# Performance work log

Hardware: AMD Instinct MI355X
Metric: run time of the kernel (lower is better)

The kernel has to match this reference:

```python
import jax, jax.numpy as jnp
from jax import lax
import numpy as np

GAMMA = 1.0
N, M = 4096, 4096


def setup_inputs() -> dict:
    key = jax.random.key(0)
    D = jax.random.normal(key, (N, M), dtype=jnp.float32)
    return {"D": D}


def reference(D):
    # Faithful translation of the original forward.
    # Step 1: the module overwrites D with exp(-D/gamma); the DP then runs on E.
    E = jnp.exp(-D / GAMMA)  # [N, M]

    # Step 2: hard-min DP (torch.min, despite the "Soft" name):
    #   c[i,j] = E[i,j] + min(c[i-1,j], c[i,j-1], c[i-1,j-1])
    # Row-wise vectorization: within row i, with a[j] = min(prev[j], prev[j-1])
    # (a[0] = prev[0]), the within-row recursion c[j] = E[j] + min(a[j], c[j-1])
    # unrolls to   c[j] = S[j] + cummin(a - S_shift)[j],  S = cumsum(E_row).
    row0 = jnp.cumsum(E[0])  # first row: pure left-to-right accumulation

    def step(prev, e_row):
        a = jnp.minimum(prev, jnp.concatenate([prev[:1], prev[:-1]]))
        S = jnp.cumsum(e_row)
        Sm1 = jnp.concatenate([jnp.zeros((1,), e_row.dtype), S[:-1]])
        c = S + lax.cummin(a - Sm1)
        return c, None

    last_row, _ = lax.scan(step, row0, E[1:])
    cost = last_row[-1]  # acc_cost[N-1, M-1]

    # Step 3: acc_grad. In the original row-major loop, acc_grad[i,j] is still 0
    # when cell (i,j) is processed (all writers come later), so each cell
    # simply (a) subtracts d[i,j]/gamma from itself and (b) adds d[i,j]/gamma to
    # its (i-1,j-1), (i-1,j), (i,j-1) neighbors, with d = exp(-E/gamma).
    # Fully vectorizable as a shifted stencil:
    d = jnp.exp(-E / GAMMA)
    dp = jnp.pad(d, ((0, 1), (0, 1)))  # zero-pad bottom/right for boundary cells
    acc_grad = (dp[1:, 1:] + dp[1:, :-1] + dp[:-1, 1:] - d) / GAMMA

    return cost, acc_grad
```

## Files before the change

kernel.cpp:

```cpp
#include <hip/hip_runtime.h>
#include <math.h>

#define NN 4096
#define STRIPS 32
#define SW 128
#define RING_ROWS 256
#define RINGB (RING_ROWS * SW * 4)
#define BATCH 32
#define NBATCH 130
#define PAD 64
#define COLPITCH (NN + 2 * PAD)
#define INFV 1e30f
#define SENTU 0xFFFFFFFFu

__device__ __forceinline__ float dpp_wave_shr1(float x) {
    return __int_as_float(__builtin_amdgcn_update_dpp(
        0, __float_as_int(x), 0x138 , 0xf, 0xf, false));
}

__device__ __forceinline__ float bload(const unsigned* colL, int row, int lane) {
    float v = INFV;
    const int rowc = (row < NN) ? row : (NN - 1);
    if (lane < 32) {
        unsigned u = __hip_atomic_load(colL + rowc, __ATOMIC_RELAXED,
                                       __HIP_MEMORY_SCOPE_AGENT);
        v = __uint_as_float(u);
    }
    return v;
}

__device__ __forceinline__ bool has_sent(float b, int rb, int lane) {
    return __any((lane < 32) && ((rb + lane) < NN) &&
                 (__float_as_uint(b) == SENTU));
}

__device__ __forceinline__ void stageB(const float* Sg, float* ring, int rb,
                                       int lane) {
    #pragma unroll
    for (int k = 0; k < 16; ++k) {
        const int r0 = rb + 2 * k;
        const int r0c = (r0 < NN - 1) ? r0 : (NN - 2);
        const int slot = r0 & (RING_ROWS - 1);
        const float* gsrc =
            Sg + (size_t)(r0c + (lane >> 5)) * NN + ((lane & 31) << 2);
        __builtin_amdgcn_global_load_lds(
            (const __attribute__((address_space(1))) unsigned*)gsrc,
            (__attribute__((address_space(3))) unsigned*)((char*)ring +
                                                         slot * (SW * 4)),
            16, 0, 0);
    }
}

template <int DOEXP>
__global__ __launch_bounds__(128, 1) void dtw_dp(const float* __restrict__ S,
                                                 float* __restrict__ cost_out,
                                                 unsigned* __restrict__ colbuf) {
    __shared__ float ring[RING_ROWS * SW];
    __shared__ float inbox[2][32];
    __shared__ float outbox[2][32];
    __shared__ float outdummy[64];

    const int tid = threadIdx.x;
    const int lane = tid & 63;
    const int b = blockIdx.x;
    const int g = ((b & 7) << 2) | (b >> 3);

    const float* Sg = S + g * SW;
    const unsigned* colL = colbuf + (size_t)(g - 1) * COLPITCH + PAD;
    unsigned* colM = colbuf + (size_t)g * COLPITCH + PAD;

    if (tid < 64) {
        {
            const float4 z = make_float4(0.f, 0.f, 0.f, 0.f);
            float4* r4 = reinterpret_cast<float4*>(&ring[192 * SW]);
            #pragma unroll
            for (int i = 0; i < 32; ++i) r4[i * 64 + lane] = z;
        }
        asm volatile("s_waitcnt lgkmcnt(0)" ::: "memory");
        __builtin_amdgcn_s_barrier();

        const bool lane0 = (lane == 0);
        const int ostep = (lane == 63) ? 1 : 0;
        float cur0 = INFV, cur1 = INFV;
        float l1s = INFV, l2s = INFV;
        float bprevc = INFV;
        float save = 0.f;

        unsigned caddr = ((unsigned)((0 - lane) & (RING_ROWS - 1)) << 9) |
                         ((unsigned)lane << 3);

        float2 rvA[BATCH], rvB[BATCH];
        #pragma unroll
        for (int s = 0; s < BATCH; ++s)
            rvA[s] = *reinterpret_cast<const float2*>(
                (const char*)ring + ((caddr + s * 512) & (RINGB - 1)));

#define CSTEP(CUR, NXT, NIDX) do {                                            \
        const int n_ = (NIDX);                                                \
        const float binb = inbox[n_ & 1][lane & 31];                          \
        _Pragma("unroll")                                                     \
        for (int s = 0; s < BATCH; ++s)                                       \
            NXT[s] = *reinterpret_cast<const float2*>(                        \
                (const char*)ring +                                           \
                ((caddr + 16384u + (unsigned)(s * 512)) & (RINGB - 1)));      \
        __builtin_amdgcn_sched_barrier(0);                                    \
        float* obp = (lane == 63) ? &outbox[n_ & 1][0] : &outdummy[lane];     \
        float pbc = INFV;                                                     \
        _Pragma("unroll")                                                     \
        for (int s = 0; s < BATCH; ++s) {                                     \
            float e0, e1;                                                     \
            if (DOEXP) { e0 = __expf(-CUR[s].x); e1 = __expf(-CUR[s].y); }    \
            else       { e0 = CUR[s].x;          e1 = CUR[s].y; }             \
            float bcur;                                                       \
            if (g == 0)                                                       \
                bcur = (n_ == 0 && s == 0) ? 0.f : INFV;                      \
            else                                                              \
                bcur = __int_as_float(                                        \
                    __builtin_amdgcn_readlane(__float_as_int(binb), s));      \
            const float bpv =                                                 \
                (g == 0) ? INFV : ((s == 0) ? bprevc : pbc);                  \
            const float L1 = lane0 ? bcur : l1s;                              \
            const float L2 = lane0 ? bpv : l2s;                               \
            const float m0 = fminf(fminf(L1, cur0), L2);                      \
            const float c0 = e0 + m0;                                         \
            const float c1 = e1 + fminf(c0, fminf(cur0, cur1));               \
            *obp = c1;                                                        \
            obp += ostep;                                                     \
            const float sh = dpp_wave_shr1(c1);                               \
            l2s = l1s; l1s = sh;                                              \
            cur0 = c0; cur1 = c1;                                             \
            pbc = bcur;                                                       \
            if (s == 30) save = c1;                                           \
        }                                                                     \
        bprevc = pbc;                                                         \
        caddr = (caddr + 16384u) & (RINGB - 1);                               \
        asm volatile("s_waitcnt lgkmcnt(0)" ::: "memory");                    \
        __builtin_amdgcn_s_barrier();                                         \
    } while (0)

        for (int i = 0; i < NBATCH / 2; ++i) {
            CSTEP(rvA, rvB, 2 * i);
            CSTEP(rvB, rvA, 2 * i + 1);
        }
#undef CSTEP

        if (g == STRIPS - 1 && lane == 63) cost_out[0] = save;
    } else {
        stageB(Sg, ring, 0, lane);
        stageB(Sg, ring, 32, lane);
        float qv = INFV;
        if (g > 0) {
            qv = bload(colL, lane & 31, lane);
            while (has_sent(qv, 0, lane)) qv = bload(colL, lane & 31, lane);
            if (lane < 32) inbox[0][lane] = qv;
            qv = bload(colL, 32 + (lane & 31), lane);
        }
        asm volatile("s_waitcnt vmcnt(0) lgkmcnt(0)" ::: "memory");
        __builtin_amdgcn_s_barrier();

        for (int n = 0; n < NBATCH; ++n) {
            const int tb = n << 5;
            if (g > 0) {
                const int vb = tb + 32;
                while (has_sent(qv, vb, lane))
                    qv = bload(colL, vb + (lane & 31), lane);
                if (lane < 32) inbox[(n + 1) & 1][lane] = qv;
                qv = bload(colL, tb + 64 + (lane & 31), lane);
            }
            if (n > 0 && lane < 32) {
                const int row = ((n - 1) << 5) - 63 + lane;
                __hip_atomic_store(colM + row,
                                   __float_as_uint(outbox[(n - 1) & 1][lane]),
                                   __ATOMIC_RELAXED, __HIP_MEMORY_SCOPE_AGENT);
            }
            stageB(Sg, ring, tb + 64, lane);
            __builtin_amdgcn_sched_barrier(0);
            if (g > 0) asm volatile("s_waitcnt vmcnt(18)" ::: "memory");
            else       asm volatile("s_waitcnt vmcnt(17)" ::: "memory");
            __builtin_amdgcn_sched_barrier(0);
            asm volatile("s_waitcnt lgkmcnt(0)" ::: "memory");
            __builtin_amdgcn_s_barrier();
        }
        if (lane < 32) {
            const int row = ((NBATCH - 1) << 5) - 63 + lane;
            __hip_atomic_store(colM + row,
                               __float_as_uint(outbox[(NBATCH - 1) & 1][lane]),
                               __ATOMIC_RELAXED, __HIP_MEMORY_SCOPE_AGENT);
        }
    }
}

__global__ __launch_bounds__(256) void eg_kernel(const float* __restrict__ D,
                                                 float* __restrict__ E,
                                                 float* __restrict__ G) {
    const int idx = blockIdx.x * 256 + threadIdx.x;
    const int i = idx >> 10;
    const int j = (idx & 1023) << 2;
    if (i >= NN) return;

    const float* row0 = D + (size_t)i * NN + j;
    const bool hasR = (i + 1) < NN;
    const bool hasC = (j + 4) < NN;

    const float4 r0 = *reinterpret_cast<const float4*>(row0);
    float4 r1 = make_float4(0.f, 0.f, 0.f, 0.f);
    if (hasR) r1 = *reinterpret_cast<const float4*>(row0 + NN);
    const float s0 = hasC ? row0[4] : 0.f;
    const float s1 = (hasR && hasC) ? row0[NN + 4] : 0.f;

    const float ex0 = __expf(-r0.x), ex1 = __expf(-r0.y);
    const float ex2 = __expf(-r0.z), ex3 = __expf(-r0.w);
    *reinterpret_cast<float4*>(E + (size_t)i * NN + j) =
        make_float4(ex0, ex1, ex2, ex3);

    const float a0 = __expf(-ex0), a1 = __expf(-ex1);
    const float a2 = __expf(-ex2), a3 = __expf(-ex3);
    const float a4 = hasC ? __expf(-__expf(-s0)) : 0.f;
    const float b0 = hasR ? __expf(-__expf(-r1.x)) : 0.f;
    const float b1 = hasR ? __expf(-__expf(-r1.y)) : 0.f;
    const float b2 = hasR ? __expf(-__expf(-r1.z)) : 0.f;
    const float b3 = hasR ? __expf(-__expf(-r1.w)) : 0.f;
    const float b4 = (hasR && hasC) ? __expf(-__expf(-s1)) : 0.f;

    float* go = G + (size_t)i * NN + j;
    go[0] = b1 + b0 + a1 - a0;
    go[1] = b2 + b1 + a2 - a1;
    go[2] = b3 + b2 + a3 - a2;
    go[3] = b4 + b3 + a4 - a3;
}

__device__ __forceinline__ float dfun(float x) { return __expf(-__expf(-x)); }

__global__ __launch_bounds__(256) void dtw_grad_kernel(const float* __restrict__ D,
                                                       float* __restrict__ G) {
    const int idx = blockIdx.x * 256 + threadIdx.x;
    const int i = idx >> 10;
    const int j = (idx & 1023) << 2;
    if (i >= NN) return;

    const float* row0 = D + (size_t)i * NN + j;
    const bool hasR = (i + 1) < NN;
    const bool hasC = (j + 4) < NN;

    const float4 r0 = *reinterpret_cast<const float4*>(row0);
    float4 r1 = make_float4(0.f, 0.f, 0.f, 0.f);
    if (hasR) r1 = *reinterpret_cast<const float4*>(row0 + NN);
    const float s0 = hasC ? row0[4] : 0.f;
    const float s1 = (hasR && hasC) ? row0[NN + 4] : 0.f;

    const float a0 = dfun(r0.x), a1 = dfun(r0.y), a2 = dfun(r0.z), a3 = dfun(r0.w);
    const float a4 = hasC ? dfun(s0) : 0.f;
    const float b0 = hasR ? dfun(r1.x) : 0.f;
    const float b1 = hasR ? dfun(r1.y) : 0.f;
    const float b2 = hasR ? dfun(r1.z) : 0.f;
    const float b3 = hasR ? dfun(r1.w) : 0.f;
    const float b4 = (hasR && hasC) ? dfun(s1) : 0.f;

    float* go = G + (size_t)i * NN + j;
    go[0] = b1 + b0 + a1 - a0;
    go[1] = b2 + b1 + a2 - a1;
    go[2] = b3 + b2 + a3 - a2;
    go[3] = b4 + b3 + a4 - a3;
}

extern "C" void kernel_launch(void* const* d_in, const int* in_sizes, int n_in,
                              void* d_out, int out_size, void* d_ws, size_t ws_size,
                              hipStream_t stream) {
    (void)in_sizes; (void)n_in; (void)out_size;
    const float* D = (const float*)d_in[0];
    float* out = (float*)d_out;

    const size_t colbytes = (size_t)STRIPS * COLPITCH * sizeof(unsigned);
    const size_t ebytes = (size_t)NN * NN * sizeof(float);
    const int gblocks = (NN * (NN / 4)) / 256;

    if (ws_size >= ebytes + colbytes) {
        float* E = (float*)d_ws;
        unsigned* colbuf = (unsigned*)((char*)d_ws + ebytes);
        hipMemsetAsync(colbuf, 0xFF, colbytes, stream);
        eg_kernel<<<gblocks, 256, 0, stream>>>(D, E, out + 1);
        dtw_dp<0><<<STRIPS, 128, 0, stream>>>(E, out, colbuf);
    } else {
        unsigned* colbuf = (ws_size >= colbytes) ? (unsigned*)d_ws
                                                 : (unsigned*)(out + 1);
        hipMemsetAsync(colbuf, 0xFF, colbytes, stream);
        dtw_dp<1><<<STRIPS, 128, 0, stream>>>(D, out, colbuf);
        dtw_grad_kernel<<<gblocks, 256, 0, stream>>>(D, out + 1);
    }
}
```

Before: 465.8 us.

## Stage DP tiles through registers and publish boundary column directly from compute wave

The loader wave now prefetches strip rows into register double-buffers with plain global loads and writes them into the LDS ring itself, replacing the global_load_lds direct-to-LDS path. The compute wave keeps its per-batch last-lane results in registers and lane 63 stores them straight to the global column buffer, removing the outbox LDS handoff and the one-batch publication delay. This is meant to shorten the latency of the cross-strip wavefront dependency. In exchange it adds register pressure, extra LDS write traffic from the loader, and a vmcnt wait in the compute loop.

```diff
diff --git a/kernel.cpp b/kernel.cpp
--- a/kernel.cpp
+++ b/kernel.cpp
@@ -34,31 +34,12 @@
                  (__float_as_uint(b) == SENTU));
 }
 
-__device__ __forceinline__ void stageB(const float* Sg, float* ring, int rb,
-                                       int lane) {
-    #pragma unroll
-    for (int k = 0; k < 16; ++k) {
-        const int r0 = rb + 2 * k;
-        const int r0c = (r0 < NN - 1) ? r0 : (NN - 2);
-        const int slot = r0 & (RING_ROWS - 1);
-        const float* gsrc =
-            Sg + (size_t)(r0c + (lane >> 5)) * NN + ((lane & 31) << 2);
-        __builtin_amdgcn_global_load_lds(
-            (const __attribute__((address_space(1))) unsigned*)gsrc,
-            (__attribute__((address_space(3))) unsigned*)((char*)ring +
-                                                         slot * (SW * 4)),
-            16, 0, 0);
-    }
-}
-
 template <int DOEXP>
 __global__ __launch_bounds__(128, 1) void dtw_dp(const float* __restrict__ S,
                                                  float* __restrict__ cost_out,
                                                  unsigned* __restrict__ colbuf) {
     __shared__ float ring[RING_ROWS * SW];
     __shared__ float inbox[2][32];
-    __shared__ float outbox[2][32];
-    __shared__ float outdummy[64];
 
     const int tid = threadIdx.x;
     const int lane = tid & 63;
@@ -80,11 +61,11 @@
         __builtin_amdgcn_s_barrier();
 
         const bool lane0 = (lane == 0);
-        const int ostep = (lane == 63) ? 1 : 0;
         float cur0 = INFV, cur1 = INFV;
         float l1s = INFV, l2s = INFV;
         float bprevc = INFV;
         float save = 0.f;
+        float csave[BATCH];
 
         unsigned caddr = ((unsigned)((0 - lane) & (RING_ROWS - 1)) << 9) |
                          ((unsigned)lane << 3);
@@ -93,10 +74,11 @@
         #pragma unroll
         for (int s = 0; s < BATCH; ++s)
             rvA[s] = *reinterpret_cast<const float2*>(
-                (const char*)ring + ((caddr + s * 512) & (RINGB - 1)));
+                (const char*)ring + ((caddr + (unsigned)(s * 512)) & (RINGB - 1)));
 
 #define CSTEP(CUR, NXT, NIDX) do {                                            \
         const int n_ = (NIDX);                                                \
+        const int tb_ = n_ << 5;                                              \
         const float binb = inbox[n_ & 1][lane & 31];                          \
         _Pragma("unroll")                                                     \
         for (int s = 0; s < BATCH; ++s)                                       \
@@ -104,7 +86,6 @@
                 (const char*)ring +                                           \
                 ((caddr + 16384u + (unsigned)(s * 512)) & (RINGB - 1)));      \
         __builtin_amdgcn_sched_barrier(0);                                    \
-        float* obp = (lane == 63) ? &outbox[n_ & 1][0] : &outdummy[lane];     \
         float pbc = INFV;                                                     \
         _Pragma("unroll")                                                     \
         for (int s = 0; s < BATCH; ++s) {                                     \
@@ -124,8 +105,7 @@
             const float m0 = fminf(fminf(L1, cur0), L2);                      \
             const float c0 = e0 + m0;                                         \
             const float c1 = e1 + fminf(c0, fminf(cur0, cur1));               \
-            *obp = c1;                                                        \
-            obp += ostep;                                                     \
+            csave[s] = c1;                                                    \
             const float sh = dpp_wave_shr1(c1);                               \
             l2s = l1s; l1s = sh;                                              \
             cur0 = c0; cur1 = c1;                                             \
@@ -134,7 +114,15 @@
         }                                                                     \
         bprevc = pbc;                                                         \
         caddr = (caddr + 16384u) & (RINGB - 1);                               \
-        asm volatile("s_waitcnt lgkmcnt(0)" ::: "memory");                    \
+        asm volatile("s_waitcnt vmcnt(32)" ::: "memory");                     \
+        if (lane == 63) {                                                     \
+            _Pragma("unroll")                                                 \
+            for (int s = 0; s < BATCH; ++s)                                   \
+                __hip_atomic_store(colM + (tb_ - 63 + s),                     \
+                                   __float_as_uint(csave[s]),                 \
+                                   __ATOMIC_RELAXED,                          \
+                                   __HIP_MEMORY_SCOPE_AGENT);                 \
+        }                                                                     \
         __builtin_amdgcn_s_barrier();                                         \
     } while (0)
 
@@ -146,8 +134,32 @@
 
         if (g == STRIPS - 1 && lane == 63) cost_out[0] = save;
     } else {
-        stageB(Sg, ring, 0, lane);
-        stageB(Sg, ring, 32, lane);
+        float4 regA[16], regB[16];
+        const int lrow = lane >> 5;
+        const int lcol = (lane & 31) << 2;
+
+        #pragma unroll
+        for (int k = 0; k < 16; ++k)
+            regA[k] = *reinterpret_cast<const float4*>(
+                Sg + (size_t)(2 * k + lrow) * NN + lcol);
+        #pragma unroll
+        for (int k = 0; k < 16; ++k)
+            regB[k] = *reinterpret_cast<const float4*>(
+                Sg + (size_t)(32 + 2 * k + lrow) * NN + lcol);
+        asm volatile("s_waitcnt vmcnt(0)" ::: "memory");
+        #pragma unroll
+        for (int k = 0; k < 16; ++k)
+            *reinterpret_cast<float4*>((char*)ring +
+                ((2 * k + lrow) << 9) + ((lane & 31) << 4)) = regA[k];
+        #pragma unroll
+        for (int k = 0; k < 16; ++k)
+            *reinterpret_cast<float4*>((char*)ring +
+                ((32 + 2 * k + lrow) << 9) + ((lane & 31) << 4)) = regB[k];
+        #pragma unroll
+        for (int k = 0; k < 16; ++k)
+            regA[k] = *reinterpret_cast<const float4*>(
+                Sg + (size_t)(64 + 2 * k + lrow) * NN + lcol);
+
         float qv = INFV;
         if (g > 0) {
             qv = bload(colL, lane & 31, lane);
@@ -155,38 +167,46 @@
             if (lane < 32) inbox[0][lane] = qv;
             qv = bload(colL, 32 + (lane & 31), lane);
         }
-        asm volatile("s_waitcnt vmcnt(0) lgkmcnt(0)" ::: "memory");
+        asm volatile("s_waitcnt lgkmcnt(0)" ::: "memory");
         __builtin_amdgcn_s_barrier();
 
-        for (int n = 0; n < NBATCH; ++n) {
-            const int tb = n << 5;
-            if (g > 0) {
-                const int vb = tb + 32;
-                while (has_sent(qv, vb, lane))
-                    qv = bload(colL, vb + (lane & 31), lane);
-                if (lane < 32) inbox[(n + 1) & 1][lane] = qv;
-                qv = bload(colL, tb + 64 + (lane & 31), lane);
-            }
-            if (n > 0 && lane < 32) {
-                const int row = ((n - 1) << 5) - 63 + lane;
-                __hip_atomic_store(colM + row,
-                                   __float_as_uint(outbox[(n - 1) & 1][lane]),
-                                   __ATOMIC_RELAXED, __HIP_MEMORY_SCOPE_AGENT);
-            }
-            stageB(Sg, ring, tb + 64, lane);
-            __builtin_amdgcn_sched_barrier(0);
-            if (g > 0) asm volatile("s_waitcnt vmcnt(18)" ::: "memory");
-            else       asm volatile("s_waitcnt vmcnt(17)" ::: "memory");
-            __builtin_amdgcn_sched_barrier(0);
-            asm volatile("s_waitcnt lgkmcnt(0)" ::: "memory");
-            __builtin_amdgcn_s_barrier();
+#define SBATCH(WR, LD, NIDX) do {                                             \
+        const int n_ = (NIDX);                                                \
+        const int tb_ = n_ << 5;                                              \
+        _Pragma("unroll")                                                     \
+        for (int k = 0; k < 16; ++k) {                                        \
+            int r0 = tb_ + 96 + 2 * k;                                        \
+            if (r0 > NN - 2) r0 = NN - 2;                                     \
+            LD[k] = *reinterpret_cast<const float4*>(                         \
+                Sg + (size_t)(r0 + lrow) * NN + lcol);                        \
+        }                                                                     \
+        __builtin_amdgcn_sched_barrier(0);                                    \
+        asm volatile("s_waitcnt vmcnt(16)" ::: "memory");                     \
+        __builtin_amdgcn_sched_barrier(0);                                    \
+        _Pragma("unroll")                                                     \
+        for (int k = 0; k < 16; ++k) {                                        \
+            const int row = tb_ + 64 + 2 * k + lrow;                          \
+            const unsigned wb =                                               \
+                ((unsigned)(row & (RING_ROWS - 1)) << 9) |                    \
+                ((unsigned)(lane & 31) << 4);                                 \
+            *reinterpret_cast<float4*>((char*)ring + wb) = WR[k];             \
+        }                                                                     \
+        if (g > 0) {                                                          \
+            const int vb = tb_ + 32;                                          \
+            while (has_sent(qv, vb, lane))                                    \
+                qv = bload(colL, vb + (lane & 31), lane);                     \
+            if (lane < 32) inbox[(n_ + 1) & 1][lane] = qv;                    \
+            qv = bload(colL, tb_ + 64 + (lane & 31), lane);                   \
+        }                                                                     \
+        asm volatile("s_waitcnt lgkmcnt(0)" ::: "memory");                    \
+        __builtin_amdgcn_s_barrier();                                         \
+    } while (0)
+
+        for (int i = 0; i < NBATCH / 2; ++i) {
+            SBATCH(regA, regB, 2 * i);
+            SBATCH(regB, regA, 2 * i + 1);
         }
-        if (lane < 32) {
-            const int row = ((NBATCH - 1) << 5) - 63 + lane;
-            __hip_atomic_store(colM + row,
-                               __float_as_uint(outbox[(NBATCH - 1) & 1][lane]),
-                               __ATOMIC_RELAXED, __HIP_MEMORY_SCOPE_AGENT);
-        }
+#undef SBATCH
     }
 }
 
```

Measured after the change: 609.6 us. 1.31x slower.

## Double DP batch to 64 rows and publish boundary column from compute wave

Applied to the files above, without the earlier changes.

Raises the per-barrier batch from 32 to 64 rows, which halves the number of block barriers and cross-strip handoffs. The producer wave now stages 64 rows ahead and polls 64-entry boundary chunks using all lanes. The compute wave writes its boundary column to global itself right after each batch instead of handing it to the producer wave one batch later. Register double-buffering of ring reads is dropped in favour of a single 64-entry load per batch, which raises register pressure and exposes LDS load latency. The larger batch also delays when downstream strips can start.

```diff
diff --git a/kernel.cpp b/kernel.cpp
--- a/kernel.cpp
+++ b/kernel.cpp
@@ -6,8 +6,8 @@
 #define SW 128
 #define RING_ROWS 256
 #define RINGB (RING_ROWS * SW * 4)
-#define BATCH 32
-#define NBATCH 130
+#define BATCH 64
+#define NBATCH 65
 #define PAD 64
 #define COLPITCH (NN + 2 * PAD)
 #define INFV 1e30f
@@ -18,26 +18,21 @@
         0, __float_as_int(x), 0x138 , 0xf, 0xf, false));
 }
 
-__device__ __forceinline__ float bload(const unsigned* colL, int row, int lane) {
-    float v = INFV;
+__device__ __forceinline__ float bload(const unsigned* colL, int row) {
     const int rowc = (row < NN) ? row : (NN - 1);
-    if (lane < 32) {
-        unsigned u = __hip_atomic_load(colL + rowc, __ATOMIC_RELAXED,
-                                       __HIP_MEMORY_SCOPE_AGENT);
-        v = __uint_as_float(u);
-    }
-    return v;
+    unsigned u = __hip_atomic_load(colL + rowc, __ATOMIC_RELAXED,
+                                   __HIP_MEMORY_SCOPE_AGENT);
+    return __uint_as_float(u);
 }
 
 __device__ __forceinline__ bool has_sent(float b, int rb, int lane) {
-    return __any((lane < 32) && ((rb + lane) < NN) &&
-                 (__float_as_uint(b) == SENTU));
+    return __any(((rb + lane) < NN) && (__float_as_uint(b) == SENTU));
 }
 
 __device__ __forceinline__ void stageB(const float* Sg, float* ring, int rb,
                                        int lane) {
     #pragma unroll
-    for (int k = 0; k < 16; ++k) {
+    for (int k = 0; k < 32; ++k) {
         const int r0 = rb + 2 * k;
         const int r0c = (r0 < NN - 1) ? r0 : (NN - 2);
         const int slot = r0 & (RING_ROWS - 1);
@@ -56,8 +51,8 @@
                                                  float* __restrict__ cost_out,
                                                  unsigned* __restrict__ colbuf) {
     __shared__ float ring[RING_ROWS * SW];
-    __shared__ float inbox[2][32];
-    __shared__ float outbox[2][32];
+    __shared__ float inbox[2][BATCH];
+    __shared__ float outbox[BATCH];
     __shared__ float outdummy[64];
 
     const int tid = threadIdx.x;
@@ -89,103 +84,88 @@
         unsigned caddr = ((unsigned)((0 - lane) & (RING_ROWS - 1)) << 9) |
                          ((unsigned)lane << 3);
 
-        float2 rvA[BATCH], rvB[BATCH];
-        #pragma unroll
-        for (int s = 0; s < BATCH; ++s)
-            rvA[s] = *reinterpret_cast<const float2*>(
-                (const char*)ring + ((caddr + s * 512) & (RINGB - 1)));
-
-#define CSTEP(CUR, NXT, NIDX) do {                                            \
-        const int n_ = (NIDX);                                                \
-        const float binb = inbox[n_ & 1][lane & 31];                          \
-        _Pragma("unroll")                                                     \
-        for (int s = 0; s < BATCH; ++s)                                       \
-            NXT[s] = *reinterpret_cast<const float2*>(                        \
-                (const char*)ring +                                           \
-                ((caddr + 16384u + (unsigned)(s * 512)) & (RINGB - 1)));      \
-        __builtin_amdgcn_sched_barrier(0);                                    \
-        float* obp = (lane == 63) ? &outbox[n_ & 1][0] : &outdummy[lane];     \
-        float pbc = INFV;                                                     \
-        _Pragma("unroll")                                                     \
-        for (int s = 0; s < BATCH; ++s) {                                     \
-            float e0, e1;                                                     \
-            if (DOEXP) { e0 = __expf(-CUR[s].x); e1 = __expf(-CUR[s].y); }    \
-            else       { e0 = CUR[s].x;          e1 = CUR[s].y; }             \
-            float bcur;                                                       \
-            if (g == 0)                                                       \
-                bcur = (n_ == 0 && s == 0) ? 0.f : INFV;                      \
-            else                                                              \
-                bcur = __int_as_float(                                        \
-                    __builtin_amdgcn_readlane(__float_as_int(binb), s));      \
-            const float bpv =                                                 \
-                (g == 0) ? INFV : ((s == 0) ? bprevc : pbc);                  \
-            const float L1 = lane0 ? bcur : l1s;                              \
-            const float L2 = lane0 ? bpv : l2s;                               \
-            const float m0 = fminf(fminf(L1, cur0), L2);                      \
-            const float c0 = e0 + m0;                                         \
-            const float c1 = e1 + fminf(c0, fminf(cur0, cur1));               \
-            *obp = c1;                                                        \
-            obp += ostep;                                                     \
-            const float sh = dpp_wave_shr1(c1);                               \
-            l2s = l1s; l1s = sh;                                              \
-            cur0 = c0; cur1 = c1;                                             \
-            pbc = bcur;                                                       \
-            if (s == 30) save = c1;                                           \
-        }                                                                     \
-        bprevc = pbc;                                                         \
-        caddr = (caddr + 16384u) & (RINGB - 1);                               \
-        asm volatile("s_waitcnt lgkmcnt(0)" ::: "memory");                    \
-        __builtin_amdgcn_s_barrier();                                         \
-    } while (0)
-
-        for (int i = 0; i < NBATCH / 2; ++i) {
-            CSTEP(rvA, rvB, 2 * i);
-            CSTEP(rvB, rvA, 2 * i + 1);
-        }
-#undef CSTEP
+        for (int n = 0; n < NBATCH; ++n) {
+            const int tb = n << 6;
+            const float binb = inbox[n & 1][lane];
+
+            float2 rv[BATCH];
+            #pragma unroll
+            for (int s = 0; s < BATCH; ++s)
+                rv[s] = *reinterpret_cast<const float2*>(
+                    (const char*)ring +
+                    ((caddr + (unsigned)(s * 512)) & (RINGB - 1)));
+
+            float* obp = (lane == 63) ? &outbox[0] : &outdummy[lane];
+            float pbc = INFV;
+            #pragma unroll
+            for (int s = 0; s < BATCH; ++s) {
+                float e0, e1;
+                if (DOEXP) { e0 = __expf(-rv[s].x); e1 = __expf(-rv[s].y); }
+                else       { e0 = rv[s].x;          e1 = rv[s].y; }
+                float bcur;
+                if (g == 0)
+                    bcur = (n == 0 && s == 0) ? 0.f : INFV;
+                else
+                    bcur = __int_as_float(
+                        __builtin_amdgcn_readlane(__float_as_int(binb), s));
+                const float bpv =
+                    (g == 0) ? INFV : ((s == 0) ? bprevc : pbc);
+                const float L1 = lane0 ? bcur : l1s;
+                const float L2 = lane0 ? bpv : l2s;
+                const float m0 = fminf(fminf(L1, cur0), L2);
+                const float c0 = e0 + m0;
+                const float c1 = e1 + fminf(c0, fminf(cur0, cur1));
+                *obp = c1;
+                obp += ostep;
+                const float sh = dpp_wave_shr1(c1);
+                l2s = l1s; l1s = sh;
+                cur0 = c0; cur1 = c1;
+                pbc = bcur;
+                if (s == 62) save = c1;
+            }
+            bprevc = pbc;
+            caddr = (caddr + (unsigned)(BATCH * 512)) & (RINGB - 1);
+
+            asm volatile("s_waitcnt lgkmcnt(0)" ::: "memory");
+            {
+                const float ob = outbox[lane];
+                asm volatile("s_waitcnt lgkmcnt(0)" ::: "memory");
+                __hip_atomic_store(colM + (tb - 63 + lane),
+                                   __float_as_uint(ob), __ATOMIC_RELAXED,
+                                   __HIP_MEMORY_SCOPE_AGENT);
+            }
+            __builtin_amdgcn_s_barrier();
+        }
 
         if (g == STRIPS - 1 && lane == 63) cost_out[0] = save;
     } else {
         stageB(Sg, ring, 0, lane);
-        stageB(Sg, ring, 32, lane);
+        stageB(Sg, ring, 64, lane);
         float qv = INFV;
         if (g > 0) {
-            qv = bload(colL, lane & 31, lane);
-            while (has_sent(qv, 0, lane)) qv = bload(colL, lane & 31, lane);
-            if (lane < 32) inbox[0][lane] = qv;
-            qv = bload(colL, 32 + (lane & 31), lane);
+            qv = bload(colL, lane);
+            while (has_sent(qv, 0, lane)) qv = bload(colL, lane);
+            inbox[0][lane] = qv;
+            qv = bload(colL, 64 + lane);
         }
         asm volatile("s_waitcnt vmcnt(0) lgkmcnt(0)" ::: "memory");
         __builtin_amdgcn_s_barrier();
 
         for (int n = 0; n < NBATCH; ++n) {
-            const int tb = n << 5;
+            const int tb = n << 6;
             if (g > 0) {
-                const int vb = tb + 32;
-                while (has_sent(qv, vb, lane))
-                    qv = bload(colL, vb + (lane & 31), lane);
-                if (lane < 32) inbox[(n + 1) & 1][lane] = qv;
-                qv = bload(colL, tb + 64 + (lane & 31), lane);
+                const int vb = tb + 64;
+                while (has_sent(qv, vb, lane)) qv = bload(colL, vb + lane);
+                inbox[(n + 1) & 1][lane] = qv;
+                qv = bload(colL, tb + 128 + lane);
             }
-            if (n > 0 && lane < 32) {
-                const int row = ((n - 1) << 5) - 63 + lane;
-                __hip_atomic_store(colM + row,
-                                   __float_as_uint(outbox[(n - 1) & 1][lane]),
-                                   __ATOMIC_RELAXED, __HIP_MEMORY_SCOPE_AGENT);
-            }
-            stageB(Sg, ring, tb + 64, lane);
+            stageB(Sg, ring, tb + 128, lane);
             __builtin_amdgcn_sched_barrier(0);
-            if (g > 0) asm volatile("s_waitcnt vmcnt(18)" ::: "memory");
-            else       asm volatile("s_waitcnt vmcnt(17)" ::: "memory");
+            if (g > 0) asm volatile("s_waitcnt vmcnt(33)" ::: "memory");
+            else       asm volatile("s_waitcnt vmcnt(32)" ::: "memory");
             __builtin_amdgcn_sched_barrier(0);
             asm volatile("s_waitcnt lgkmcnt(0)" ::: "memory");
             __builtin_amdgcn_s_barrier();
-        }
-        if (lane < 32) {
-            const int row = ((NBATCH - 1) << 5) - 63 + lane;
-            __hip_atomic_store(colM + row,
-                               __float_as_uint(outbox[(NBATCH - 1) & 1][lane]),
-                               __ATOMIC_RELAXED, __HIP_MEMORY_SCOPE_AGENT);
         }
     }
 }
```

New measurement: 491.6 us. +5.5%, slower.
